# Kernel tuning notes

Hardware: AMD Instinct MI355X
Metric: run time of the kernel (lower is better)

## Reference

```python
import jax, jax.numpy as jnp
import numpy as np

B, C_IN, MID, H, W = 4, 512, 512, 50, 50
A = 9
FEAT_STRIDE = 16
IMG = H * FEAT_STRIDE  # 800
N_PRE, N_POST = 1200, 300
NMS_TH = 0.7
MIN_SIZE = 16.0


def _anchor_base(base=16.0, ratios=(0.5, 1.0, 2.0), scales=(8, 16, 32)):
    ab = np.zeros((len(ratios) * len(scales), 4), np.float32)
    py = px = base / 2.0
    for i, r in enumerate(ratios):
        for j, s in enumerate(scales):
            h = base * s * np.sqrt(r)
            w = base * s * np.sqrt(1.0 / r)
            ab[i * len(scales) + j] = [py - h / 2, px - w / 2, py + h / 2, px + w / 2]
    return ab


def _all_anchors():
    ab = _anchor_base()
    sy = np.arange(0, H * FEAT_STRIDE, FEAT_STRIDE, dtype=np.float32)
    sx = np.arange(0, W * FEAT_STRIDE, FEAT_STRIDE, dtype=np.float32)
    SX, SY = np.meshgrid(sx, sy)
    shift = np.stack([SY.ravel(), SX.ravel(), SY.ravel(), SX.ravel()], axis=1)
    return jnp.asarray((shift[:, None, :] + ab[None]).reshape(-1, 4))  # [H*W*A,4]


ANCHORS = _all_anchors()


def _conv(x, w, b, pad):
    y = jax.lax.conv_general_dilated(x, w, (1, 1), [(pad, pad), (pad, pad)],
                                     dimension_numbers=('NCHW', 'OIHW', 'NCHW'))
    return y + b[None, :, None, None]


def _loc2bbox(anc, loc):
    h = anc[:, 2] - anc[:, 0]
    w = anc[:, 3] - anc[:, 1]
    cy = anc[:, 0] + 0.5 * h
    cx = anc[:, 1] + 0.5 * w
    dy, dx, dh, dw = loc[:, 0], loc[:, 1], loc[:, 2], loc[:, 3]
    ncy = dy * h + cy
    ncx = dx * w + cx
    nh = jnp.exp(dh) * h
    nw = jnp.exp(dw) * w
    return jnp.stack([ncy - 0.5 * nh, ncx - 0.5 * nw, ncy + 0.5 * nh, ncx + 0.5 * nw], axis=1)


def _nms_keep(boxes, thresh):
    y1, x1, y2, x2 = boxes[:, 0], boxes[:, 1], boxes[:, 2], boxes[:, 3]
    iy = jnp.clip(jnp.minimum(y2[:, None], y2[None]) - jnp.maximum(y1[:, None], y1[None]), 0.0)
    ix = jnp.clip(jnp.minimum(x2[:, None], x2[None]) - jnp.maximum(x1[:, None], x1[None]), 0.0)
    inter = iy * ix
    area = (y2 - y1) * (x2 - x1)
    iou = inter / (area[:, None] + area[None] - inter + 1e-9)  # [N_PRE,N_PRE]

    def step(carry, i):
        sup, keep = carry
        k = ~sup[i]
        keep = keep.at[i].set(k)
        newsup = jnp.where(k & (iou[i] > thresh), True, sup)
        newsup = newsup.at[i].set(sup[i])
        return (newsup, keep), None

    n = boxes.shape[0]
    init = (jnp.zeros(n, bool), jnp.zeros(n, bool))
    (_, keep), _ = jax.lax.scan(step, init, jnp.arange(n))
    return keep


def _propose(loc, fg):
    roi = _loc2bbox(ANCHORS, loc)
    roi = jnp.stack([jnp.clip(roi[:, 0], 0.0, IMG), jnp.clip(roi[:, 1], 0.0, IMG),
                     jnp.clip(roi[:, 2], 0.0, IMG), jnp.clip(roi[:, 3], 0.0, IMG)], axis=1)
    hs = roi[:, 2] - roi[:, 0]
    ws = roi[:, 3] - roi[:, 1]
    s = jnp.where((hs >= MIN_SIZE) & (ws >= MIN_SIZE), fg, -jnp.inf)
    top_s, top_i = jax.lax.top_k(s, N_PRE)          # score-sorted pre-NMS candidates
    boxes = roi[top_i]
    keep = _nms_keep(boxes, NMS_TH)
    _, sel = jax.lax.top_k(jnp.where(keep, top_s, -jnp.inf), N_POST)
    return boxes[sel]                                # [N_POST,4]


def setup_inputs() -> dict:
    key = jax.random.key(0)
    ks = jax.random.split(key, 4)
    x = jax.random.normal(ks[0], (B, C_IN, H, W), jnp.float32)
    W1 = jax.random.normal(ks[1], (MID, C_IN, 3, 3), jnp.float32) * 0.01
    b1 = jnp.zeros((MID,), jnp.float32)
    Wl = jax.random.normal(ks[2], (A * 4, MID, 1, 1), jnp.float32) * 0.01
    bl = jnp.zeros((A * 4,), jnp.float32)
    Ws = jax.random.normal(ks[3], (A * 2, MID, 1, 1), jnp.float32) * 0.01
    bs = jnp.zeros((A * 2,), jnp.float32)
    return {'x': x, 'W1': W1, 'b1': b1, 'Wl': Wl, 'bl': bl, 'Ws': Ws, 'bs': bs}


def reference(x, W1, b1, Wl, bl, Ws, bs):
    h = jax.nn.relu(_conv(x, W1, b1, 1))
    locs = _conv(h, Wl, bl, 0)     # [B, A*4, H, W]
    scores = _conv(h, Ws, bs, 0)   # [B, A*2, H, W]
    rpn_locs = locs.transpose(0, 2, 3, 1).reshape(B, -1, 4)          # [B, H*W*A, 4]
    sc = scores.transpose(0, 2, 3, 1).reshape(B, H, W, A, 2)
    fg = jax.nn.softmax(sc, axis=-1)[..., 1].reshape(B, -1)          # [B, H*W*A]
    rpn_scores = sc.reshape(B, -1, 2)
    rois = jax.vmap(_propose)(rpn_locs, fg)                          # [B, N_POST, 4]
    return rpn_locs, rpn_scores, rois
```

## Files before the change

### kernel.cpp

```cpp
#include <hip/hip_runtime.h>
#include <math.h>

#define BATCH 4
#define CIN 512
#define MID 512
#define HH 50
#define WW 50
#define HWPIX 2500
#define NPIX 10000
#define NANCH 22500
#define NPRE 1200
#define NPOST 300
#define LOCS_OFF 0
#define SCORES_OFF 360000
#define ROIS_OFF 540000

#define PADW 52
#define PPIX 2704

typedef _Float16 half8 __attribute__((ext_vector_type(8)));
typedef float floatx4 __attribute__((ext_vector_type(4)));

__device__ __forceinline__ void gload16(const void* g, void* l) {
    __builtin_amdgcn_global_load_lds(
        (const __attribute__((address_space(1))) unsigned int*)g,
        (__attribute__((address_space(3))) unsigned int*)l, 16, 0, 0);
}

__device__ __forceinline__ unsigned long long rdlane64(unsigned int lo,
                                                       unsigned int hi, int l) {
    const unsigned int a = (unsigned int)__builtin_amdgcn_readlane((int)lo, l);
    const unsigned int b = (unsigned int)__builtin_amdgcn_readlane((int)hi, l);
    return ((unsigned long long)b << 32) | a;
}


__global__ __launch_bounds__(256) void prep_x_kernel(
    const float* __restrict__ x, _Float16* __restrict__ xh,
    _Float16* __restrict__ xl) {
    __shared__ float tile[64][65];
    const int t  = threadIdx.x;
    const int pt = blockIdx.x;
    const int ct = blockIdx.y;
    const int b  = blockIdx.z;
    const int p0 = pt * 64, c0 = ct * 64;

    #pragma unroll
    for (int r = 0; r < 16; ++r) {
        const int cc = (t >> 6) + r * 4;
        const int pp = t & 63;
        const int p  = p0 + pp;
        tile[cc][pp] = (p < HWPIX) ? x[((size_t)b * 512 + c0 + cc) * HWPIX + p] : 0.f;
    }
    __syncthreads();
    #pragma unroll
    for (int r = 0; r < 16; ++r) {
        const int pp = (t >> 6) + r * 4;
        const int cc = t & 63;
        const int p  = p0 + pp;
        if (p < HWPIX) {
            const int y = p / WW, xx2 = p % WW;
            const float v = tile[cc][pp];
            const _Float16 hh = (_Float16)v;
            const float rr = v - (float)hh;
            const _Float16 ll = (_Float16)(rr * 2048.0f);
            const size_t o = ((size_t)(b * PPIX + (y + 1) * PADW + xx2 + 1)) * 512 + c0 + cc;
            xh[o] = hh;
            xl[o] = ll;
        }
    }
}

__global__ __launch_bounds__(256) void prep_w_kernel(
    const float* __restrict__ W1, const float* __restrict__ Wl,
    const float* __restrict__ Wsc, _Float16* __restrict__ wth,
    _Float16* __restrict__ wtl, float* __restrict__ wh,
    _Float16* __restrict__ xh, _Float16* __restrict__ xl) {
    __shared__ float buf[4608];
    const int blk = blockIdx.x;
    const int t   = threadIdx.x;
    if (blk < 512) {
        const int m = blk;
        const float* src = W1 + (size_t)m * 4608;
        for (int i = t; i < 4608; i += 256) buf[i] = src[i];
        __syncthreads();
        for (int kk = 0; kk < 9; ++kk) {
            for (int c = t; c < 512; c += 256) {
                const float v = buf[c * 9 + kk];
                const _Float16 hh = (_Float16)v;
                const float rr = v - (float)hh;
                const size_t o = (size_t)kk * 262144 + (size_t)m * 512 + c;
                wth[o] = hh;
                wtl[o] = (_Float16)(rr * 2048.0f);
            }
        }
    } else if (blk < 640) {
        const int g2 = (blk - 512) * 256 + t;
        const int c = g2 >> 6, n = g2 & 63;
        float v = 0.f;
        if (n < 36)      v = Wl[n * 512 + c];
        else if (n < 54) v = Wsc[(n - 36) * 512 + c];
        wh[g2] = v;
    } else {
        const int idx = (blk - 640) * 256 + t;
        if (idx < BATCH * PPIX * 4) {
            const int pix = idx >> 2, q = idx & 3;
            const int r = pix % PPIX;
            const int yy = r / PADW, xx2 = r % PADW;
            if (yy == 0 || yy == PADW - 1 || xx2 == 0 || xx2 == PADW - 1) {
                float4 z = make_float4(0.f, 0.f, 0.f, 0.f);
                float4* ph = (float4*)(xh + (size_t)pix * 512 + q * 128);
                float4* pl = (float4*)(xl + (size_t)pix * 512 + q * 128);
                #pragma unroll
                for (int i = 0; i < 16; ++i) { ph[i] = z; pl[i] = z; }
            }
        }
    }
}

#define BUFSZ 24576
#define AOFF_L 8192
#define BOFF_H 16384
#define BOFF_L 20480
#define MTILES 80

__global__ __launch_bounds__(256) void conv_mfma_kernel(
    const _Float16* __restrict__ xh, const _Float16* __restrict__ xl,
    const _Float16* __restrict__ wth, const _Float16* __restrict__ wtl,
    const float* __restrict__ b1, float* __restrict__ h) {
    __shared__ __align__(16) char lds[2 * BUFSZ];

    const int bid  = blockIdx.x;
    const int t    = threadIdx.x;
    const int w    = t >> 6;
    const int lane = t & 63;
    const int n0   = (bid / MTILES) * 64;
    const int m0   = (bid % MTILES) * 128;
    const int wq   = w * 1024;

    const int sr = t >> 2;
    const int cp = t & 3;
    const int clA = (cp - (sr >> 1)) & 3;
    const int clB = clA;

    int P0 = m0 + sr;       if (P0 > NPIX - 1) P0 = NPIX - 1;
    int P1 = m0 + sr + 64;  if (P1 > NPIX - 1) P1 = NPIX - 1;
    const int b0 = P0 / HWPIX, pl0 = P0 % HWPIX;
    const int b1i = P1 / HWPIX, pl1 = P1 % HWPIX;
    const int baseA0 = ((b0 * PPIX) + (pl0 / WW + 1) * PADW + (pl0 % WW + 1)) * 512 + clA * 8;
    const int baseA1 = ((b1i * PPIX) + (pl1 / WW + 1) * PADW + (pl1 % WW + 1)) * 512 + clA * 8;
    const int baseB  = (n0 + sr) * 512 + clB * 8;

    const int lr = lane & 15, lq = lane >> 4;
    const int wrow = w * 32;
    const int rA0 = wrow + lr, rA1 = wrow + 16 + lr;
    const int offA0 = rA0 * 64 + (((lq + (rA0 >> 1)) & 3) << 4);
    const int offA1 = rA1 * 64 + (((lq + (rA1 >> 1)) & 3) << 4);
    int offB[4];
    #pragma unroll
    for (int ctl = 0; ctl < 4; ++ctl) {
        const int rB = ctl * 16 + lr;
        offB[ctl] = rB * 64 + (((lq + (rB >> 1)) & 3) << 4);
    }

    floatx4 acc1[2][4] = {};
    floatx4 acc2[2][4] = {};

    auto issue = [&](int u) {
        char* D = lds + ((u & 1) ? BUFSZ : 0);
        const int kk = u >> 4, ct = u & 15;
        const int kd = kk / 3;
        const int dA = ((kd - 1) * PADW + (kk - kd * 3 - 1)) * 512 + ct * 32;
        const int dB = kk * 262144 + ct * 32;
        gload16(xh + baseA0 + dA, D + 0 + wq);
        gload16(xh + baseA1 + dA, D + 4096 + wq);
        gload16(xl + baseA0 + dA, D + AOFF_L + wq);
        gload16(xl + baseA1 + dA, D + AOFF_L + 4096 + wq);
        gload16(wth + baseB + dB, D + BOFF_H + wq);
        gload16(wtl + baseB + dB, D + BOFF_L + wq);
    };

    issue(0);
    for (int s = 0; s < 144; ++s) {
        __syncthreads();
        if (s + 1 < 144) issue(s + 1);
        const char* Bb = lds + ((s & 1) ? BUFSZ : 0);
        const half8 afh0 = *(const half8*)(Bb + offA0);
        const half8 afh1 = *(const half8*)(Bb + offA1);
        const half8 afl0 = *(const half8*)(Bb + AOFF_L + offA0);
        const half8 afl1 = *(const half8*)(Bb + AOFF_L + offA1);
        #pragma unroll
        for (int ctl = 0; ctl < 4; ++ctl) {
            const half8 bfh = *(const half8*)(Bb + BOFF_H + offB[ctl]);
            const half8 bfl = *(const half8*)(Bb + BOFF_L + offB[ctl]);
            acc1[0][ctl] = __builtin_amdgcn_mfma_f32_16x16x32_f16(afh0, bfh, acc1[0][ctl], 0, 0, 0);
            acc2[0][ctl] = __builtin_amdgcn_mfma_f32_16x16x32_f16(afh0, bfl, acc2[0][ctl], 0, 0, 0);
            acc2[0][ctl] = __builtin_amdgcn_mfma_f32_16x16x32_f16(afl0, bfh, acc2[0][ctl], 0, 0, 0);
            acc1[1][ctl] = __builtin_amdgcn_mfma_f32_16x16x32_f16(afh1, bfh, acc1[1][ctl], 0, 0, 0);
            acc2[1][ctl] = __builtin_amdgcn_mfma_f32_16x16x32_f16(afh1, bfl, acc2[1][ctl], 0, 0, 0);
            acc2[1][ctl] = __builtin_amdgcn_mfma_f32_16x16x32_f16(afl1, bfh, acc2[1][ctl], 0, 0, 0);
        }
    }

    const float s2 = 1.0f / 2048.0f;
    #pragma unroll
    for (int rt = 0; rt < 2; ++rt) {
        #pragma unroll
        for (int ctl = 0; ctl < 4; ++ctl) {
            const int m = n0 + ctl * 16 + lr;
            const float bias = b1[m];
            #pragma unroll
            for (int r = 0; r < 4; ++r) {
                const int P = m0 + wrow + rt * 16 + lq * 4 + r;
                if (P < NPIX) {
                    const float v = acc1[rt][ctl][r] + acc2[rt][ctl][r] * s2 + bias;
                    h[(size_t)P * 512 + m] = fmaxf(v, 0.f);
                }
            }
        }
    }
}

__global__ void wt_kernel(const float* __restrict__ W1,
                          const float* __restrict__ Wl,
                          const float* __restrict__ Wsc,
                          float* __restrict__ w1t, float* __restrict__ wh) {
    int g = blockIdx.x * 256 + threadIdx.x;
    if (g < 9 * 512 * 512) {
        int kk = g / (512 * 512);
        int r  = g % (512 * 512);
        int c  = r / 512;
        int m  = r % 512;
        w1t[g] = W1[(size_t)m * 4608 + c * 9 + kk];
    } else {
        int g2 = g - 9 * 512 * 512;
        if (g2 < 512 * 64) {
            int c = g2 >> 6, n = g2 & 63;
            float v = 0.f;
            if (n < 36)      v = Wl[n * 512 + c];
            else if (n < 54) v = Wsc[(n - 36) * 512 + c];
            wh[g2] = v;
        }
    }
}

__global__ __launch_bounds__(256) void conv3x3_fallback(
    const float* __restrict__ x, const float* __restrict__ w1t,
    const float* __restrict__ b1, float* __restrict__ h) {
    __shared__ float As[16][64];
    __shared__ float Bs[16][64];
    const int t  = threadIdx.x;
    const int tx = t & 15;
    const int ty = t >> 4;
    const int m0 = blockIdx.x * 64;
    const int n0 = blockIdx.y * 64;
    const int pix = t & 63;
    const int cl0 = t >> 6;
    const int P  = m0 + pix;
    const bool vp = (P < NPIX);
    const int b  = P / HWPIX;
    const int pl = P % HWPIX;
    const int yy = pl / WW;
    const int xx = pl % WW;
    float acc[4][4] = {};
    for (int kk = 0; kk < 9; ++kk) {
        const int ky = kk / 3 - 1, kx = kk % 3 - 1;
        const int y2 = yy + ky, x2 = xx + kx;
        const bool v = vp && ((unsigned)y2 < (unsigned)HH) && ((unsigned)x2 < (unsigned)WW);
        const float* xbase = x + (size_t)b * CIN * HWPIX + y2 * WW + x2;
        const float* wbase = w1t + (size_t)kk * 512 * 512 + n0;
        for (int ct = 0; ct < 512 / 16; ++ct) {
            __syncthreads();
            #pragma unroll
            for (int r = 0; r < 4; ++r) {
                const int cl = cl0 + r * 4;
                const int c  = ct * 16 + cl;
                As[cl][pix] = v ? xbase[(size_t)c * HWPIX] : 0.f;
                Bs[cl][pix] = wbase[c * 512 + pix];
            }
            __syncthreads();
            #pragma unroll
            for (int k = 0; k < 16; ++k) {
                const float4 a4 = *reinterpret_cast<const float4*>(&As[k][ty * 4]);
                const float4 b4 = *reinterpret_cast<const float4*>(&Bs[k][tx * 4]);
                const float av[4] = {a4.x, a4.y, a4.z, a4.w};
                const float bv[4] = {b4.x, b4.y, b4.z, b4.w};
                #pragma unroll
                for (int i = 0; i < 4; ++i)
                    #pragma unroll
                    for (int j = 0; j < 4; ++j)
                        acc[i][j] = fmaf(av[i], bv[j], acc[i][j]);
            }
        }
    }
    #pragma unroll
    for (int i = 0; i < 4; ++i) {
        const int Pp = m0 + ty * 4 + i;
        if (Pp >= NPIX) continue;
        const int m = n0 + tx * 4;
        float4 o;
        o.x = fmaxf(acc[i][0] + b1[m + 0], 0.f);
        o.y = fmaxf(acc[i][1] + b1[m + 1], 0.f);
        o.z = fmaxf(acc[i][2] + b1[m + 2], 0.f);
        o.w = fmaxf(acc[i][3] + b1[m + 3], 0.f);
        *reinterpret_cast<float4*>(&h[(size_t)Pp * 512 + m]) = o;
    }
}


__global__ __launch_bounds__(256) void heads_kernel(
    const float* __restrict__ h, const float* __restrict__ wh,
    const float* __restrict__ bl, const float* __restrict__ bsc,
    float* __restrict__ out, float* __restrict__ fgb) {
    __shared__ float As[16][17];
    __shared__ float Bs[16][64];
    const int t  = threadIdx.x;
    const int p  = t & 15;
    const int g  = t >> 4;
    const int p0 = blockIdx.x * 16;

    float acc[4] = {0.f, 0.f, 0.f, 0.f};

    for (int ct = 0; ct < 32; ++ct) {
        const int c0 = ct * 16;
        __syncthreads();
        {
            const int pp = t >> 4, cc = t & 15;
            const int PP = p0 + pp;
            As[cc][pp] = (PP < NPIX) ? h[(size_t)PP * 512 + c0 + cc] : 0.f;
            #pragma unroll
            for (int r = 0; r < 4; ++r) {
                const int row = (t >> 6) + 4 * r;
                Bs[row][t & 63] = wh[(size_t)(c0 + row) * 64 + (t & 63)];
            }
        }
        __syncthreads();
        #pragma unroll
        for (int k = 0; k < 16; ++k) {
            const float a = As[k][p];
            const float4 b4 = *reinterpret_cast<const float4*>(&Bs[k][g * 4]);
            acc[0] = fmaf(a, b4.x, acc[0]);
            acc[1] = fmaf(a, b4.y, acc[1]);
            acc[2] = fmaf(a, b4.z, acc[2]);
            acc[3] = fmaf(a, b4.w, acc[3]);
        }
    }

    const int P = p0 + p;
    if (P >= NPIX) return;
    const int b  = P / HWPIX;
    const int pl = P % HWPIX;
    const int n  = g * 4;
    const size_t abase = (size_t)b * NANCH + (size_t)pl * 9;
    if (n < 36) {
        const int a = g;
        float4 o;
        o.x = acc[0] + bl[n + 0];
        o.y = acc[1] + bl[n + 1];
        o.z = acc[2] + bl[n + 2];
        o.w = acc[3] + bl[n + 3];
        *reinterpret_cast<float4*>(&out[LOCS_OFF + (abase + a) * 4]) = o;
    } else if (n < 54) {
        const int ns = n - 36;
        float* so = out + SCORES_OFF;
        {
            const float s0 = acc[0] + bsc[ns + 0];
            const float s1 = acc[1] + bsc[ns + 1];
            const int a0 = ns >> 1;
            so[(abase + a0) * 2 + 0] = s0;
            so[(abase + a0) * 2 + 1] = s1;
            const float mx = fmaxf(s0, s1);
            const float e0 = expf(s0 - mx);
            const float e1 = expf(s1 - mx);
            fgb[abase + a0] = e1 / (e0 + e1);
        }
        if (ns + 3 < 18) {
            const float s0 = acc[2] + bsc[ns + 2];
            const float s1 = acc[3] + bsc[ns + 3];
            const int a1 = (ns >> 1) + 1;
            so[(abase + a1) * 2 + 0] = s0;
            so[(abase + a1) * 2 + 1] = s1;
            const float mx = fmaxf(s0, s1);
            const float e0 = expf(s0 - mx);
            const float e1 = expf(s1 - mx);
            fgb[abase + a1] = e1 / (e0 + e1);
        }
    }
}

__global__ void proposal_prep(const float* __restrict__ out,
                              const float* __restrict__ fgb,
                              float* __restrict__ roi_all,
                              unsigned long long* __restrict__ keys) {
    #pragma clang fp contract(off)
    const int j = blockIdx.x * 256 + threadIdx.x;
    const int b = blockIdx.y;
    if (j >= NANCH) return;

    const int a = j % 9;
    const int p = j / 9;
    const int y = p / WW;
    const int x = p % WW;
    const int ri = a / 3, si = a % 3;
    const double rr[3] = {0.5, 1.0, 2.0};
    const double ss[3] = {8.0, 16.0, 32.0};
    const double hh = 16.0 * ss[si] * sqrt(rr[ri]);
    const double wd = 16.0 * ss[si] * sqrt(1.0 / rr[ri]);
    const float ab0 = (float)(8.0 - hh / 2.0);
    const float ab1 = (float)(8.0 - wd / 2.0);
    const float ab2 = (float)(8.0 + hh / 2.0);
    const float ab3 = (float)(8.0 + wd / 2.0);
    const float sy = (float)(y * 16);
    const float sx = (float)(x * 16);
    const float ay1 = sy + ab0;
    const float ax1 = sx + ab1;
    const float ay2 = sy + ab2;
    const float ax2 = sx + ab3;

    const float h  = ay2 - ay1;
    const float w  = ax2 - ax1;
    const float cy = ay1 + 0.5f * h;
    const float cx = ax1 + 0.5f * w;

    const float* L = out + LOCS_OFF + ((size_t)b * NANCH + j) * 4;
    const float dy = L[0], dx = L[1], dh = L[2], dw = L[3];

    const float ncy = dy * h + cy;
    const float ncx = dx * w + cx;
    const float nh  = expf(dh) * h;
    const float nw  = expf(dw) * w;

    float r0 = ncy - 0.5f * nh;
    float r1 = ncx - 0.5f * nw;
    float r2 = ncy + 0.5f * nh;
    float r3 = ncx + 0.5f * nw;
    r0 = fminf(fmaxf(r0, 0.f), 800.f);
    r1 = fminf(fmaxf(r1, 0.f), 800.f);
    r2 = fminf(fmaxf(r2, 0.f), 800.f);
    r3 = fminf(fmaxf(r3, 0.f), 800.f);

    const float hs  = r2 - r0;
    const float wsz = r3 - r1;
    const float fg  = fgb[(size_t)b * NANCH + j];
    const float s   = (hs >= 16.f && wsz >= 16.f) ? fg : -__builtin_huge_valf();

    float4 ro;
    ro.x = r0; ro.y = r1; ro.z = r2; ro.w = r3;
    *reinterpret_cast<float4*>(&roi_all[((size_t)b * NANCH + j) * 4]) = ro;

    unsigned int bits = __float_as_uint(s);
    unsigned int o = (bits & 0x80000000u) ? ~bits : (bits | 0x80000000u);
    keys[(size_t)b * NANCH + j] =
        ((unsigned long long)o << 32) | (unsigned int)(~(unsigned int)j);
}

__global__ __launch_bounds__(1024) void select_sort_kernel(
    const unsigned long long* __restrict__ keys,
    const float* __restrict__ roi_all, float* __restrict__ boxes) {
    const int b   = blockIdx.x;
    const int tid = threadIdx.x;
    const unsigned long long* K = keys + (size_t)b * NANCH;

    __shared__ unsigned int hist[256][4];
    __shared__ unsigned int suf[256];
    __shared__ unsigned long long sbuf[2048];
    __shared__ unsigned int prefix_s;
    __shared__ int rank_s;
    __shared__ int cnt_s;

    const int sub = (tid >> 8) & 3;

    if (tid == 0) { prefix_s = 0u; rank_s = NPRE; }
    __syncthreads();

    for (int pass = 0; pass < 4; ++pass) {
        for (int i = tid; i < 1024; i += 1024) ((unsigned int*)hist)[i] = 0;
        __syncthreads();
        const unsigned pref = prefix_s;
        for (int i = tid; i < NANCH; i += 1024) {
            const unsigned hk = (unsigned)(K[i] >> 32);
            const bool match = (pass == 0) || ((hk >> (32 - 8 * pass)) == pref);
            if (match) atomicAdd(&hist[(hk >> (24 - 8 * pass)) & 255u][sub], 1u);
        }
        __syncthreads();
        if (tid < 256)
            suf[tid] = hist[tid][0] + hist[tid][1] + hist[tid][2] + hist[tid][3];
        __syncthreads();
        for (int st = 1; st < 256; st <<= 1) {
            unsigned v = 0;
            if (tid < 256) v = suf[tid] + ((tid + st < 256) ? suf[tid + st] : 0u);
            __syncthreads();
            if (tid < 256) suf[tid] = v;
            __syncthreads();
        }
        const int r = rank_s;
        __syncthreads();
        if (tid < 256) {
            const unsigned s_here = suf[tid];
            const unsigned s_up   = (tid < 255) ? suf[tid + 1] : 0u;
            if (s_here >= (unsigned)r && s_up < (unsigned)r) {
                rank_s = r - (int)s_up;
                prefix_s = (prefix_s << 8) | (unsigned)tid;
            }
        }
        __syncthreads();
    }

    const unsigned kth32 = prefix_s;
    if (tid == 0) cnt_s = 0;
    __syncthreads();
    for (int i = tid; i < NANCH; i += 1024) {
        const unsigned long long k = K[i];
        if ((unsigned)(k >> 32) >= kth32) {
            const int p = atomicAdd(&cnt_s, 1);
            if (p < 2048) sbuf[p] = k;
        }
    }
    __syncthreads();
    const int cnt = cnt_s;
    for (int i = tid; i < 2048; i += 1024)
        if (i >= cnt) sbuf[i] = 0ULL;

    for (int ksz = 2; ksz <= 2048; ksz <<= 1) {
        for (int jj = ksz >> 1; jj > 0; jj >>= 1) {
            __syncthreads();
            for (int i = tid; i < 2048; i += 1024) {
                const int l = i ^ jj;
                if (l > i) {
                    const unsigned long long a = sbuf[i];
                    const unsigned long long c = sbuf[l];
                    const bool asc = (i & ksz) != 0;
                    const bool sw  = asc ? (a > c) : (a < c);
                    if (sw) { sbuf[i] = c; sbuf[l] = a; }
                }
            }
        }
    }
    __syncthreads();

    for (int r = tid; r < NPRE; r += 1024) {
        const unsigned long long k = sbuf[r];
        const unsigned int idx = ~((unsigned int)k);
        const float4 v = *reinterpret_cast<const float4*>(
            &roi_all[((size_t)b * NANCH + idx) * 4]);
        *reinterpret_cast<float4*>(&boxes[((size_t)b * NPRE + r) * 4]) = v;
    }
}

__global__ __launch_bounds__(64) void iou_kernel(
    const float* __restrict__ boxes, unsigned long long* __restrict__ mask) {
    #pragma clang fp contract(off)
    const int rb = blockIdx.x;
    const int b  = blockIdx.y;
    const int t  = threadIdx.x;
    __shared__ float bx[NPRE * 4];
    __shared__ float ar[NPRE];

    for (int i = t; i < NPRE * 4; i += 64)
        bx[i] = boxes[(size_t)b * NPRE * 4 + i];
    __syncthreads();
    for (int i = t; i < NPRE; i += 64)
        ar[i] = (bx[i * 4 + 2] - bx[i * 4 + 0]) * (bx[i * 4 + 3] - bx[i * 4 + 1]);
    __syncthreads();

    const int i = rb * 64 + t;
    if (i >= NPRE) return;
    const float y1 = bx[i * 4 + 0], x1 = bx[i * 4 + 1];
    const float y2 = bx[i * 4 + 2], x2 = bx[i * 4 + 3];
    const float ai = ar[i];
    for (int jw = 0; jw < 19; ++jw) {
        unsigned long long bits = 0ULL;
        const int jmax = (jw * 64 + 64 <= NPRE) ? 64 : (NPRE - jw * 64);
        for (int jb = 0; jb < jmax; ++jb) {
            const int j = jw * 64 + jb;
            const float iy = fmaxf(fminf(y2, bx[j * 4 + 2]) - fmaxf(y1, bx[j * 4 + 0]), 0.f);
            const float ix = fmaxf(fminf(x2, bx[j * 4 + 3]) - fmaxf(x1, bx[j * 4 + 1]), 0.f);
            const float inter = iy * ix;
            const float den = ((ai + ar[j]) - inter) + 1e-9f;
            const float iou = inter / den;
            if (iou > 0.7f) bits |= (1ULL << jb);
        }
        mask[((size_t)b * NPRE + i) * 19 + jw] = bits;
    }
}

__global__ __launch_bounds__(64) void nms_scan_kernel(
    const unsigned long long* __restrict__ mask,
    const float* __restrict__ boxes, float* __restrict__ out_rois) {
    const int b    = blockIdx.x;
    const int lane = threadIdx.x;
    const unsigned long long* M = mask + (size_t)b * NPRE * 19;

    __shared__ unsigned long long tile[2][1216];
    __shared__ unsigned long long kw[19];
    __shared__ int sel[NPOST];

    const int lw = (lane < 19) ? lane : 0;

    {
        unsigned long long pre[19];
        #pragma unroll
        for (int q = 0; q < 19; ++q) pre[q] = M[q * 64 + lane];
        #pragma unroll
        for (int q = 0; q < 19; ++q) tile[0][q * 64 + lane] = pre[q];
    }
    __syncthreads();

    unsigned long long sup = 0ULL;

    for (int w = 0; w < 19; ++w) {
        const int cur = w & 1;
        unsigned long long pre[19];
        if (w + 1 < 19) {
            const int gb = (w + 1) * 1216;
            #pragma unroll
            for (int q = 0; q < 19; ++q) pre[q] = M[gb + q * 64 + lane];
        }

        const int nrows = (w == 18) ? (NPRE - 18 * 64) : 64;
        const unsigned long long* tp = tile[cur];

        const unsigned long long diag = (lane < nrows) ? tp[lane * 19 + w] : 0ULL;
        const unsigned int dlo = (unsigned int)diag;
        const unsigned int dhi = (unsigned int)(diag >> 32);

        const unsigned long long ext =
            rdlane64((unsigned int)sup, (unsigned int)(sup >> 32), w);

        unsigned long long sup_in = ext, keep = 0ULL;
        for (int i = 0; i < nrows; ++i) {
            const unsigned long long di = rdlane64(dlo, dhi, i);
            if (!((sup_in >> i) & 1ULL)) {
                keep |= (1ULL << i);
                sup_in |= di;
            }
        }

        #pragma unroll
        for (int i = 0; i < 64; ++i) {
            const unsigned long long mi = tp[i * 19 + lw];
            sup |= mi & (0ULL - ((keep >> i) & 1ULL));
        }

        if (lane == 0) kw[w] = keep;

        if (w + 1 < 19) {
            #pragma unroll
            for (int q = 0; q < 19; ++q) tile[1 - cur][q * 64 + lane] = pre[q];
        }
        __syncthreads();
    }

    int total = 0;
    #pragma unroll
    for (int w = 0; w < 19; ++w) total += __popcll(kw[w]);

    int pref = 0;
    #pragma unroll
    for (int w = 0; w < 19; ++w) {
        const unsigned long long kwv = kw[w];
        const int i = w * 64 + lane;
        const int kr = pref + __popcll(kwv & ((1ULL << lane) - 1ULL));
        if (i < NPRE) {
            if ((kwv >> lane) & 1ULL) {
                if (kr < NPOST) sel[kr] = i;
            } else {
                const int r2 = total + (i - kr);
                if (r2 < NPOST) sel[r2] = i;
            }
        }
        pref += __popcll(kwv);
    }
    __syncthreads();

    for (int rr = lane; rr < NPOST; rr += 64) {
        const int i = sel[rr];
        const float4 v = *reinterpret_cast<const float4*>(
            &boxes[((size_t)b * NPRE + i) * 4]);
        *reinterpret_cast<float4*>(&out_rois[((size_t)b * NPOST + rr) * 4]) = v;
    }
}

extern "C" void kernel_launch(void* const* d_in, const int* in_sizes, int n_in,
                              void* d_out, int out_size, void* d_ws, size_t ws_size,
                              hipStream_t stream) {
    const float* x   = (const float*)d_in[0];
    const float* W1  = (const float*)d_in[1];
    const float* b1  = (const float*)d_in[2];
    const float* Wl  = (const float*)d_in[3];
    const float* bl  = (const float*)d_in[4];
    const float* Wsc = (const float*)d_in[5];
    const float* bsc = (const float*)d_in[6];
    float* out = (float*)d_out;
    char* ws = (char*)d_ws;

    const size_t MAIN_BYTES = 52199424ULL;

    if (ws_size >= MAIN_BYTES) {
        float*    h    = (float*)(ws);
        _Float16* xh   = (_Float16*)(ws + 20480000);
        _Float16* xl   = (_Float16*)(ws + 31555584);
        _Float16* wth  = (_Float16*)(ws + 42631168);
        _Float16* wtl  = (_Float16*)(ws + 47349760);
        float*    wh   = (float*)(ws + 52068352);
        char* alias = ws + 20480000;
        float* fgb  = (float*)(alias);
        float* roi  = (float*)(alias + 360000);
        unsigned long long* keys = (unsigned long long*)(alias + 1800000);
        float* boxes = (float*)(alias + 2520000);
        unsigned long long* mask = (unsigned long long*)(alias + 2596800);

        hipLaunchKernelGGL(prep_x_kernel, dim3(40, 8, BATCH), dim3(256), 0, stream,
                           x, xh, xl);
        hipLaunchKernelGGL(prep_w_kernel, dim3(512 + 128 + 169), dim3(256), 0, stream,
                           W1, Wl, Wsc, wth, wtl, wh, xh, xl);
        hipLaunchKernelGGL(conv_mfma_kernel, dim3(8 * MTILES), dim3(256), 0, stream,
                           xh, xl, wth, wtl, b1, h);
        hipLaunchKernelGGL(heads_kernel, dim3(625), dim3(256), 0, stream,
                           h, wh, bl, bsc, out, fgb);
        hipLaunchKernelGGL(proposal_prep, dim3((NANCH + 255) / 256, BATCH), dim3(256), 0, stream,
                           out, fgb, roi, keys);
        hipLaunchKernelGGL(select_sort_kernel, dim3(BATCH), dim3(1024), 0, stream,
                           keys, roi, boxes);
        hipLaunchKernelGGL(iou_kernel, dim3(19, BATCH), dim3(64), 0, stream,
                           boxes, mask);
        hipLaunchKernelGGL(nms_scan_kernel, dim3(BATCH), dim3(64), 0, stream,
                           mask, boxes, out + ROIS_OFF);
    } else {
        float* fws = (float*)ws;
        float* w1t     = fws;
        float* h       = w1t + 2359296;
        float* fgb     = h + 5120000;
        float* wh      = fgb + 90000;
        float* roi     = wh + 32768;
        unsigned long long* keys = (unsigned long long*)(roi + 360000);
        float* boxes   = (float*)(keys + 90000);
        unsigned long long* mask = (unsigned long long*)(boxes + 19200);

        hipLaunchKernelGGL(wt_kernel, dim3((9 * 512 * 512 + 512 * 64 + 255) / 256),
                           dim3(256), 0, stream, W1, Wl, Wsc, w1t, wh);
        hipLaunchKernelGGL(conv3x3_fallback, dim3((NPIX + 63) / 64, 512 / 64), dim3(256), 0, stream,
                           x, w1t, b1, h);
        hipLaunchKernelGGL(heads_kernel, dim3(625), dim3(256), 0, stream,
                           h, wh, bl, bsc, out, fgb);
        hipLaunchKernelGGL(proposal_prep, dim3((NANCH + 255) / 256, BATCH), dim3(256), 0, stream,
                           out, fgb, roi, keys);
        hipLaunchKernelGGL(select_sort_kernel, dim3(BATCH), dim3(1024), 0, stream,
                           keys, roi, boxes);
        hipLaunchKernelGGL(iou_kernel, dim3(19, BATCH), dim3(64), 0, stream,
                           boxes, mask);
        hipLaunchKernelGGL(nms_scan_kernel, dim3(BATCH), dim3(64), 0, stream,
                           mask, boxes, out + ROIS_OFF);
    }
}
```

Baseline: 583.6 us.

## Merge prep kernels and halve conv N-tile to double block count

The two preprocessing kernels (input transpose/split and weight split plus border zeroing) become one launch that dispatches on block index. This removes a launch and lets the weight and activation prep run concurrently. The conv MFMA kernel's output-channel tile shrinks from 64 to 32, giving 1280 blocks instead of 640 and a smaller LDS buffer, so occupancy and CU coverage should improve on a 256-CU part. In exchange, each block reuses its A tile across fewer channels, which doubles A-tile global traffic, and B loads are split across waves.

```diff
diff --git a/kernel.cpp b/kernel.cpp
--- a/kernel.cpp
+++ b/kernel.cpp
@@ -35,93 +35,94 @@
 }
 
 
-__global__ __launch_bounds__(256) void prep_x_kernel(
-    const float* __restrict__ x, _Float16* __restrict__ xh,
-    _Float16* __restrict__ xl) {
-    __shared__ float tile[64][65];
-    const int t  = threadIdx.x;
-    const int pt = blockIdx.x;
-    const int ct = blockIdx.y;
-    const int b  = blockIdx.z;
-    const int p0 = pt * 64, c0 = ct * 64;
-
-    #pragma unroll
-    for (int r = 0; r < 16; ++r) {
-        const int cc = (t >> 6) + r * 4;
-        const int pp = t & 63;
-        const int p  = p0 + pp;
-        tile[cc][pp] = (p < HWPIX) ? x[((size_t)b * 512 + c0 + cc) * HWPIX + p] : 0.f;
-    }
-    __syncthreads();
-    #pragma unroll
-    for (int r = 0; r < 16; ++r) {
-        const int pp = (t >> 6) + r * 4;
-        const int cc = t & 63;
-        const int p  = p0 + pp;
-        if (p < HWPIX) {
-            const int y = p / WW, xx2 = p % WW;
-            const float v = tile[cc][pp];
-            const _Float16 hh = (_Float16)v;
-            const float rr = v - (float)hh;
-            const _Float16 ll = (_Float16)(rr * 2048.0f);
-            const size_t o = ((size_t)(b * PPIX + (y + 1) * PADW + xx2 + 1)) * 512 + c0 + cc;
-            xh[o] = hh;
-            xl[o] = ll;
-        }
-    }
-}
-
-__global__ __launch_bounds__(256) void prep_w_kernel(
-    const float* __restrict__ W1, const float* __restrict__ Wl,
-    const float* __restrict__ Wsc, _Float16* __restrict__ wth,
-    _Float16* __restrict__ wtl, float* __restrict__ wh,
-    _Float16* __restrict__ xh, _Float16* __restrict__ xl) {
-    __shared__ float buf[4608];
+__global__ __launch_bounds__(256) void prep_combo_kernel(
+    const float* __restrict__ x, const float* __restrict__ W1,
+    const float* __restrict__ Wl, const float* __restrict__ Wsc,
+    _Float16* __restrict__ xh, _Float16* __restrict__ xl,
+    _Float16* __restrict__ wth, _Float16* __restrict__ wtl,
+    float* __restrict__ wh) {
+    __shared__ __align__(16) char smem[18432];
     const int blk = blockIdx.x;
     const int t   = threadIdx.x;
-    if (blk < 512) {
-        const int m = blk;
-        const float* src = W1 + (size_t)m * 4608;
-        for (int i = t; i < 4608; i += 256) buf[i] = src[i];
-        __syncthreads();
-        for (int kk = 0; kk < 9; ++kk) {
-            for (int c = t; c < 512; c += 256) {
-                const float v = buf[c * 9 + kk];
+
+    if (blk < 1280) {
+        float (*tile)[65] = (float(*)[65])smem;
+        const int pt = blk % 40;
+        const int ct = (blk / 40) % 8;
+        const int b  = blk / 320;
+        const int p0 = pt * 64, c0 = ct * 64;
+
+        #pragma unroll
+        for (int r = 0; r < 16; ++r) {
+            const int cc = (t >> 6) + r * 4;
+            const int pp = t & 63;
+            const int p  = p0 + pp;
+            tile[cc][pp] = (p < HWPIX) ? x[((size_t)b * 512 + c0 + cc) * HWPIX + p] : 0.f;
+        }
+        __syncthreads();
+        #pragma unroll
+        for (int r = 0; r < 16; ++r) {
+            const int pp = (t >> 6) + r * 4;
+            const int cc = t & 63;
+            const int p  = p0 + pp;
+            if (p < HWPIX) {
+                const int y = p / WW, xx2 = p % WW;
+                const float v = tile[cc][pp];
                 const _Float16 hh = (_Float16)v;
                 const float rr = v - (float)hh;
-                const size_t o = (size_t)kk * 262144 + (size_t)m * 512 + c;
-                wth[o] = hh;
-                wtl[o] = (_Float16)(rr * 2048.0f);
-            }
-        }
-    } else if (blk < 640) {
-        const int g2 = (blk - 512) * 256 + t;
-        const int c = g2 >> 6, n = g2 & 63;
-        float v = 0.f;
-        if (n < 36)      v = Wl[n * 512 + c];
-        else if (n < 54) v = Wsc[(n - 36) * 512 + c];
-        wh[g2] = v;
+                const _Float16 ll = (_Float16)(rr * 2048.0f);
+                const size_t o = ((size_t)(b * PPIX + (y + 1) * PADW + xx2 + 1)) * 512 + c0 + cc;
+                xh[o] = hh;
+                xl[o] = ll;
+            }
+        }
     } else {
-        const int idx = (blk - 640) * 256 + t;
-        if (idx < BATCH * PPIX * 4) {
-            const int pix = idx >> 2, q = idx & 3;
-            const int r = pix % PPIX;
-            const int yy = r / PADW, xx2 = r % PADW;
-            if (yy == 0 || yy == PADW - 1 || xx2 == 0 || xx2 == PADW - 1) {
-                float4 z = make_float4(0.f, 0.f, 0.f, 0.f);
-                float4* ph = (float4*)(xh + (size_t)pix * 512 + q * 128);
-                float4* pl = (float4*)(xl + (size_t)pix * 512 + q * 128);
-                #pragma unroll
-                for (int i = 0; i < 16; ++i) { ph[i] = z; pl[i] = z; }
-            }
-        }
-    }
-}
-
-#define BUFSZ 24576
+        const int wblk = blk - 1280;
+        if (wblk < 512) {
+            float* buf = (float*)smem;
+            const int m = wblk;
+            const float* src = W1 + (size_t)m * 4608;
+            for (int i = t; i < 4608; i += 256) buf[i] = src[i];
+            __syncthreads();
+            for (int kk = 0; kk < 9; ++kk) {
+                for (int c = t; c < 512; c += 256) {
+                    const float v = buf[c * 9 + kk];
+                    const _Float16 hh = (_Float16)v;
+                    const float rr = v - (float)hh;
+                    const size_t o = (size_t)kk * 262144 + (size_t)m * 512 + c;
+                    wth[o] = hh;
+                    wtl[o] = (_Float16)(rr * 2048.0f);
+                }
+            }
+        } else if (wblk < 640) {
+            const int g2 = (wblk - 512) * 256 + t;
+            const int c = g2 >> 6, n = g2 & 63;
+            float v = 0.f;
+            if (n < 36)      v = Wl[n * 512 + c];
+            else if (n < 54) v = Wsc[(n - 36) * 512 + c];
+            wh[g2] = v;
+        } else {
+            const int idx = (wblk - 640) * 256 + t;
+            if (idx < BATCH * PPIX * 4) {
+                const int pix = idx >> 2, q = idx & 3;
+                const int r = pix % PPIX;
+                const int yy = r / PADW, xx2 = r % PADW;
+                if (yy == 0 || yy == PADW - 1 || xx2 == 0 || xx2 == PADW - 1) {
+                    float4 z = make_float4(0.f, 0.f, 0.f, 0.f);
+                    float4* ph = (float4*)(xh + (size_t)pix * 512 + q * 128);
+                    float4* pl = (float4*)(xl + (size_t)pix * 512 + q * 128);
+                    #pragma unroll
+                    for (int i = 0; i < 16; ++i) { ph[i] = z; pl[i] = z; }
+                }
+            }
+        }
+    }
+}
+
+#define BUFSZ 20480
 #define AOFF_L 8192
 #define BOFF_H 16384
-#define BOFF_L 20480
+#define BOFF_L 18432
 #define MTILES 80
 
 __global__ __launch_bounds__(256) void conv_mfma_kernel(
@@ -134,14 +135,13 @@
     const int t    = threadIdx.x;
     const int w    = t >> 6;
     const int lane = t & 63;
-    const int n0   = (bid / MTILES) * 64;
+    const int n0   = (bid / MTILES) * 32;
     const int m0   = (bid % MTILES) * 128;
     const int wq   = w * 1024;
 
     const int sr = t >> 2;
     const int cp = t & 3;
     const int clA = (cp - (sr >> 1)) & 3;
-    const int clB = clA;
 
     int P0 = m0 + sr;       if (P0 > NPIX - 1) P0 = NPIX - 1;
     int P1 = m0 + sr + 64;  if (P1 > NPIX - 1) P1 = NPIX - 1;
@@ -149,22 +149,27 @@
     const int b1i = P1 / HWPIX, pl1 = P1 % HWPIX;
     const int baseA0 = ((b0 * PPIX) + (pl0 / WW + 1) * PADW + (pl0 % WW + 1)) * 512 + clA * 8;
     const int baseA1 = ((b1i * PPIX) + (pl1 / WW + 1) * PADW + (pl1 % WW + 1)) * 512 + clA * 8;
-    const int baseB  = (n0 + sr) * 512 + clB * 8;
+
+    const int wb  = (w < 2) ? w : (w - 2);
+    const int rB  = wb * 16 + (lane >> 2);
+    const int cpB = lane & 3;
+    const int clB = (cpB - (rB >> 1)) & 3;
+    const int baseB = (n0 + rB) * 512 + clB * 8;
 
     const int lr = lane & 15, lq = lane >> 4;
     const int wrow = w * 32;
     const int rA0 = wrow + lr, rA1 = wrow + 16 + lr;
     const int offA0 = rA0 * 64 + (((lq + (rA0 >> 1)) & 3) << 4);
     const int offA1 = rA1 * 64 + (((lq + (rA1 >> 1)) & 3) << 4);
-    int offB[4];
+    int offB[2];
     #pragma unroll
-    for (int ctl = 0; ctl < 4; ++ctl) {
-        const int rB = ctl * 16 + lr;
-        offB[ctl] = rB * 64 + (((lq + (rB >> 1)) & 3) << 4);
-    }
-
-    floatx4 acc1[2][4] = {};
-    floatx4 acc2[2][4] = {};
+    for (int ctl = 0; ctl < 2; ++ctl) {
+        const int rBf = ctl * 16 + lr;
+        offB[ctl] = rBf * 64 + (((lq + (rBf >> 1)) & 3) << 4);
+    }
+
+    floatx4 acc1[2][2] = {};
+    floatx4 acc2[2][2] = {};
 
     auto issue = [&](int u) {
         char* D = lds + ((u & 1) ? BUFSZ : 0);
@@ -176,8 +181,8 @@
         gload16(xh + baseA1 + dA, D + 4096 + wq);
         gload16(xl + baseA0 + dA, D + AOFF_L + wq);
         gload16(xl + baseA1 + dA, D + AOFF_L + 4096 + wq);
-        gload16(wth + baseB + dB, D + BOFF_H + wq);
-        gload16(wtl + baseB + dB, D + BOFF_L + wq);
+        if (w < 2) gload16(wth + baseB + dB, D + BOFF_H + wb * 1024);
+        else       gload16(wtl + baseB + dB, D + BOFF_L + wb * 1024);
     };
 
     issue(0);
@@ -190,7 +195,7 @@
         const half8 afl0 = *(const half8*)(Bb + AOFF_L + offA0);
         const half8 afl1 = *(const half8*)(Bb + AOFF_L + offA1);
         #pragma unroll
-        for (int ctl = 0; ctl < 4; ++ctl) {
+        for (int ctl = 0; ctl < 2; ++ctl) {
             const half8 bfh = *(const half8*)(Bb + BOFF_H + offB[ctl]);
             const half8 bfl = *(const half8*)(Bb + BOFF_L + offB[ctl]);
             acc1[0][ctl] = __builtin_amdgcn_mfma_f32_16x16x32_f16(afh0, bfh, acc1[0][ctl], 0, 0, 0);
@@ -206,7 +211,7 @@
     #pragma unroll
     for (int rt = 0; rt < 2; ++rt) {
         #pragma unroll
-        for (int ctl = 0; ctl < 4; ++ctl) {
+        for (int ctl = 0; ctl < 2; ++ctl) {
             const int m = n0 + ctl * 16 + lr;
             const float bias = b1[m];
             #pragma unroll
@@ -710,11 +715,9 @@
         float* boxes = (float*)(alias + 2520000);
         unsigned long long* mask = (unsigned long long*)(alias + 2596800);
 
-        hipLaunchKernelGGL(prep_x_kernel, dim3(40, 8, BATCH), dim3(256), 0, stream,
-                           x, xh, xl);
-        hipLaunchKernelGGL(prep_w_kernel, dim3(512 + 128 + 169), dim3(256), 0, stream,
-                           W1, Wl, Wsc, wth, wtl, wh, xh, xl);
-        hipLaunchKernelGGL(conv_mfma_kernel, dim3(8 * MTILES), dim3(256), 0, stream,
+        hipLaunchKernelGGL(prep_combo_kernel, dim3(1280 + 512 + 128 + 169), dim3(256), 0, stream,
+                           x, W1, Wl, Wsc, xh, xl, wth, wtl, wh);
+        hipLaunchKernelGGL(conv_mfma_kernel, dim3(16 * MTILES), dim3(256), 0, stream,
                            xh, xl, wth, wtl, b1, h);
         hipLaunchKernelGGL(heads_kernel, dim3(625), dim3(256), 0, stream,
                            h, wh, bl, bsc, out, fgb);
```

Result: slower. 618.6 us (+6.0%).
